# Performance work log

Hardware: AMD Instinct MI355X
Metric: run time of the kernel (lower is better)

Reference implementation:

```python
import jax, jax.numpy as jnp
import numpy as np

INV_SQRT2 = 0.7071067811865476  # db1 (Haar) filter coefficient
KEYS = ("aad", "ada", "add", "daa", "dad", "dda", "ddd")  # ptwt wavedec3 detail keys, dims (D,H,W)


def dwt1(x, axis):
    """Single-level 1D Haar DWT along `axis` (zero mode, even length -> no padding).
    lo[k] = (x[2k] + x[2k+1]) / sqrt(2), hi[k] = (x[2k] - x[2k+1]) / sqrt(2),
    matching pywt/ptwt db1 with mode='zero'."""
    ev = jax.lax.slice_in_dim(x, 0, None, stride=2, axis=axis)
    od = jax.lax.slice_in_dim(x, 1, None, stride=2, axis=axis)
    return (ev + od) * INV_SQRT2, (ev - od) * INV_SQRT2


def haar3(x):
    """One level of separable 3D Haar DWT on [B, C, D, H, W] -> dict of 8 subbands,
    each [B, C, D/2, H/2, W/2]. Key letters correspond to (D, H, W)."""
    out = {}
    aD, dD = dwt1(x, 2)
    for k0, t0 in (("a", aD), ("d", dD)):
        aH, dH = dwt1(t0, 3)
        for k1, t1 in (("a", aH), ("d", dH)):
            aW, dW = dwt1(t1, 4)
            out[k0 + k1 + "a"] = aW
            out[k0 + k1 + "d"] = dW
    return out


def wavedec3(x, level):
    """Multi-level 3D Haar wavedec (ptwt.wavedec3, wavelet='db1', mode='zero').
    Returns (Yl, [details_coarsest, ..., details_finest])."""
    details = []
    cur = x
    for _ in range(level):
        sb = haar3(cur)
        cur = sb.pop("aaa")
        details.append(sb)
    return cur, details[::-1]  # ptwt orders coarsest level first


def setup_inputs() -> dict:
    key = jax.random.key(0)
    x = jax.random.normal(key, (4, 8, 128, 128, 128), dtype=jnp.float32)
    return {"x": x, "level": 5}


def reference(x, level):
    Yl, Yh = wavedec3(x, level)
    outs = [Yl]
    for d in Yh:
        outs.extend(d[k] for k in KEYS)
    return tuple(outs)
```

## Files before the change

### kernel.cpp

```cpp
#include <hip/hip_runtime.h>


#define C3 0.3535533905932738f

typedef float f4 __attribute__((ext_vector_type(4)));

__device__ __forceinline__ f4 ntload(const float* p) {
    return __builtin_nontemporal_load((const f4*)p);
}
__device__ __forceinline__ void ntstore(float* p, f4 v) {
    __builtin_nontemporal_store(v, (f4*)p);
}

__device__ __forceinline__ void haar_quad(const float r[4][8], float o[8][4]) {
#pragma unroll
    for (int j = 0; j < 4; ++j) {
        const float aw0 = r[0][2*j] + r[0][2*j+1], dw0 = r[0][2*j] - r[0][2*j+1];
        const float aw1 = r[1][2*j] + r[1][2*j+1], dw1 = r[1][2*j] - r[1][2*j+1];
        const float aw2 = r[2][2*j] + r[2][2*j+1], dw2 = r[2][2*j] - r[2][2*j+1];
        const float aw3 = r[3][2*j] + r[3][2*j+1], dw3 = r[3][2*j] - r[3][2*j+1];
        const float aa0 = aw0 + aw1, da0 = aw0 - aw1, ad0 = dw0 + dw1, dd0 = dw0 - dw1;
        const float aa1 = aw2 + aw3, da1 = aw2 - aw3, ad1 = dw2 + dw3, dd1 = dw2 - dw3;
        o[0][j] = (aa0 + aa1) * C3;
        o[1][j] = (ad0 + ad1) * C3;
        o[2][j] = (da0 + da1) * C3;
        o[3][j] = (dd0 + dd1) * C3;
        o[4][j] = (aa0 - aa1) * C3;
        o[5][j] = (ad0 - ad1) * C3;
        o[6][j] = (da0 - da1) * C3;
        o[7][j] = (dd0 - dd1) * C3;
    }
}

__device__ __forceinline__ void lds_quad(const float* p, int dh, int dd, float r[4][8]) {
    *(f4*)&r[0][0] = *(const f4*)(p);
    *(f4*)&r[0][4] = *(const f4*)(p + 4);
    *(f4*)&r[1][0] = *(const f4*)(p + dh);
    *(f4*)&r[1][4] = *(const f4*)(p + dh + 4);
    *(f4*)&r[2][0] = *(const f4*)(p + dd);
    *(f4*)&r[2][4] = *(const f4*)(p + dd + 4);
    *(f4*)&r[3][0] = *(const f4*)(p + dd + dh);
    *(f4*)&r[3][4] = *(const f4*)(p + dd + dh + 4);
}

__global__ __launch_bounds__(512, 4) void haar3_fused(
    const float* __restrict__ in, float* __restrict__ out)
{
    __shared__ float A1[16 * 16 * 68];
    __shared__ float A2[8 * 8 * 36];
    __shared__ float A3[4 * 4 * 16];
    __shared__ float A4[2 * 2 * 8];

    const int tid = threadIdx.x;
    const int bc = blockIdx.x >> 4;
    const int db = (blockIdx.x >> 2) & 3;
    const int hb = blockIdx.x & 3;

    const float* xin = in + (((long)bc * 128 + db * 32) * 128 + hb * 32) * 128;
    float* const d1 = out + 8388608;
    float* const d2 = out + 1048576;
    float* const d3 = out + 131072;
    float* const d4 = out + 16384;
    float* const d5 = out + 2048;

    for (int it = 0; it < 8; ++it) {
        const int u = it * 512 + tid;
        const int wg = u & 15, hy = (u >> 4) & 15, dz = u >> 8;
        const float* p = xin + ((long)(2 * dz) * 128 + 2 * hy) * 128 + 8 * wg;
        float r[4][8];
        *(f4*)&r[0][0] = ntload(p);
        *(f4*)&r[0][4] = ntload(p + 4);
        *(f4*)&r[1][0] = ntload(p + 128);
        *(f4*)&r[1][4] = ntload(p + 132);
        *(f4*)&r[2][0] = ntload(p + 16384);
        *(f4*)&r[2][4] = ntload(p + 16388);
        *(f4*)&r[3][0] = ntload(p + 16512);
        *(f4*)&r[3][4] = ntload(p + 16516);
        float o[8][4];
        haar_quad(r, o);
        *(f4*)&A1[(dz * 16 + hy) * 68 + 4 * wg] = *(const f4*)&o[0][0];
        const long di = (((long)bc * 64 + db * 16 + dz) * 64 + hb * 16 + hy) * 64 + 4 * wg;
#pragma unroll
        for (int s = 0; s < 7; ++s)
            ntstore(d1 + (long)s * 8388608 + di, *(const f4*)&o[s + 1][0]);
    }
    __syncthreads();

    {
        const int wg = tid & 7, hy = (tid >> 3) & 7, dz = tid >> 6;
        float r[4][8];
        lds_quad(&A1[((2 * dz) * 16 + 2 * hy) * 68 + 8 * wg], 68, 16 * 68, r);
        float o[8][4];
        haar_quad(r, o);
        *(f4*)&A2[(dz * 8 + hy) * 36 + 4 * wg] = *(const f4*)&o[0][0];
        const long di = (((long)bc * 32 + db * 8 + dz) * 32 + hb * 8 + hy) * 32 + 4 * wg;
#pragma unroll
        for (int s = 0; s < 7; ++s)
            ntstore(d2 + (long)s * 1048576 + di, *(const f4*)&o[s + 1][0]);
    }
    __syncthreads();

    if (tid < 64) {
        const int wg = tid & 3, hy = (tid >> 2) & 3, dz = tid >> 4;
        float r[4][8];
        lds_quad(&A2[((2 * dz) * 8 + 2 * hy) * 36 + 8 * wg], 36, 8 * 36, r);
        float o[8][4];
        haar_quad(r, o);
        *(f4*)&A3[(dz * 4 + hy) * 16 + 4 * wg] = *(const f4*)&o[0][0];
        const long di = (((long)bc * 16 + db * 4 + dz) * 16 + hb * 4 + hy) * 16 + 4 * wg;
#pragma unroll
        for (int s = 0; s < 7; ++s)
            ntstore(d3 + (long)s * 131072 + di, *(const f4*)&o[s + 1][0]);
    }
    __syncthreads();

    if (tid < 8) {
        const int wg = tid & 1, hy = (tid >> 1) & 1, dz = tid >> 2;
        float r[4][8];
        lds_quad(&A3[((2 * dz) * 4 + 2 * hy) * 16 + 8 * wg], 16, 64, r);
        float o[8][4];
        haar_quad(r, o);
        *(f4*)&A4[(dz * 2 + hy) * 8 + 4 * wg] = *(const f4*)&o[0][0];
        const long di = (((long)bc * 8 + db * 2 + dz) * 8 + hb * 2 + hy) * 8 + 4 * wg;
#pragma unroll
        for (int s = 0; s < 7; ++s)
            ntstore(d4 + (long)s * 16384 + di, *(const f4*)&o[s + 1][0]);
    }
    __syncthreads();

    if (tid == 0) {
        float r[4][8];
        lds_quad(&A4[0], 8, 16, r);
        float o[8][4];
        haar_quad(r, o);
        const long di = (((long)bc * 4 + db) * 4 + hb) * 4;
        *(f4*)(out + di) = *(const f4*)&o[0][0];
#pragma unroll
        for (int s = 0; s < 7; ++s)
            *(f4*)(d5 + (long)s * 2048 + di) = *(const f4*)&o[s + 1][0];
    }
}

extern "C" void kernel_launch(void* const* d_in, const int* in_sizes, int n_in,
                              void* d_out, int out_size, void* d_ws, size_t ws_size,
                              hipStream_t stream) {
    const float* x = (const float*)d_in[0];
    float* out = (float*)d_out;
    (void)d_ws; (void)ws_size;

    haar3_fused<<<512, 512, 0, stream>>>(x, out);
}
```

Baseline: 456.6 us.

## Split blocks along W, swizzle level-1 LDS layout, and alias LDS buffers

```diff
diff --git a/kernel.cpp b/kernel.cpp
--- a/kernel.cpp
+++ b/kernel.cpp
@@ -4,6 +4,7 @@
 #define C3 0.3535533905932738f
 
 typedef float f4 __attribute__((ext_vector_type(4)));
+typedef float f2 __attribute__((ext_vector_type(2)));
 
 __device__ __forceinline__ f4 ntload(const float* p) {
     return __builtin_nontemporal_load((const f4*)p);
@@ -32,96 +33,108 @@
     }
 }
 
-__device__ __forceinline__ void lds_quad(const float* p, int dh, int dd, float r[4][8]) {
-    *(f4*)&r[0][0] = *(const f4*)(p);
-    *(f4*)&r[0][4] = *(const f4*)(p + 4);
-    *(f4*)&r[1][0] = *(const f4*)(p + dh);
-    *(f4*)&r[1][4] = *(const f4*)(p + dh + 4);
-    *(f4*)&r[2][0] = *(const f4*)(p + dd);
-    *(f4*)&r[2][4] = *(const f4*)(p + dd + 4);
-    *(f4*)&r[3][0] = *(const f4*)(p + dd + dh);
-    *(f4*)&r[3][4] = *(const f4*)(p + dd + dh + 4);
+__device__ __forceinline__ int sw1(int dz, int hy, int c4) {
+    return (dz * 16 + hy) * 32 + (c4 ^ ((((dz >> 1) ^ (hy >> 1)) & 7) << 2));
 }
 
 __global__ __launch_bounds__(512, 4) void haar3_fused(
     const float* __restrict__ in, float* __restrict__ out)
 {
-    __shared__ float A1[16 * 16 * 68];
-    __shared__ float A2[8 * 8 * 36];
-    __shared__ float A3[4 * 4 * 16];
-    __shared__ float A4[2 * 2 * 8];
+    __shared__ float A1[16 * 16 * 32];
+    __shared__ float A2[8 * 8 * 16];
+    float* const A3 = A1;
+    float* const A4 = A2;
 
     const int tid = threadIdx.x;
-    const int bc = blockIdx.x >> 4;
-    const int db = (blockIdx.x >> 2) & 3;
-    const int hb = blockIdx.x & 3;
+    const int bid = blockIdx.x;
+    const int wb = bid & 1, hb = (bid >> 1) & 3, db = (bid >> 3) & 3, bc = bid >> 5;
 
-    const float* xin = in + (((long)bc * 128 + db * 32) * 128 + hb * 32) * 128;
+    const float* xin = in + (((long)bc * 128 + db * 32) * 128 + hb * 32) * 128 + wb * 64;
     float* const d1 = out + 8388608;
     float* const d2 = out + 1048576;
     float* const d3 = out + 131072;
     float* const d4 = out + 16384;
     float* const d5 = out + 2048;
 
-    for (int it = 0; it < 8; ++it) {
+#pragma unroll 2
+    for (int it = 0; it < 4; ++it) {
         const int u = it * 512 + tid;
-        const int wg = u & 15, hy = (u >> 4) & 15, dz = u >> 8;
+        const int wg = u & 7, hy = (u >> 3) & 15, dz = u >> 7;
         const float* p = xin + ((long)(2 * dz) * 128 + 2 * hy) * 128 + 8 * wg;
         float r[4][8];
-        *(f4*)&r[0][0] = ntload(p);
-        *(f4*)&r[0][4] = ntload(p + 4);
-        *(f4*)&r[1][0] = ntload(p + 128);
-        *(f4*)&r[1][4] = ntload(p + 132);
-        *(f4*)&r[2][0] = ntload(p + 16384);
-        *(f4*)&r[2][4] = ntload(p + 16388);
-        *(f4*)&r[3][0] = ntload(p + 16512);
-        *(f4*)&r[3][4] = ntload(p + 16516);
+        *(f4*)&r[0][0] = ntload(p);         *(f4*)&r[0][4] = ntload(p + 4);
+        *(f4*)&r[1][0] = ntload(p + 128);   *(f4*)&r[1][4] = ntload(p + 132);
+        *(f4*)&r[2][0] = ntload(p + 16384); *(f4*)&r[2][4] = ntload(p + 16388);
+        *(f4*)&r[3][0] = ntload(p + 16512); *(f4*)&r[3][4] = ntload(p + 16516);
         float o[8][4];
         haar_quad(r, o);
-        *(f4*)&A1[(dz * 16 + hy) * 68 + 4 * wg] = *(const f4*)&o[0][0];
-        const long di = (((long)bc * 64 + db * 16 + dz) * 64 + hb * 16 + hy) * 64 + 4 * wg;
+        *(f4*)&A1[sw1(dz, hy, 4 * wg)] = *(const f4*)&o[0][0];
+        const long di = (((long)bc * 64 + db * 16 + dz) * 64 + hb * 16 + hy) * 64
+                        + 32 * wb + 4 * wg;
 #pragma unroll
         for (int s = 0; s < 7; ++s)
             ntstore(d1 + (long)s * 8388608 + di, *(const f4*)&o[s + 1][0]);
     }
     __syncthreads();
 
-    {
-        const int wg = tid & 7, hy = (tid >> 3) & 7, dz = tid >> 6;
+    if (tid < 256) {
+        const int wg = tid & 3, hy = (tid >> 2) & 7, dz = tid >> 5;
         float r[4][8];
-        lds_quad(&A1[((2 * dz) * 16 + 2 * hy) * 68 + 8 * wg], 68, 16 * 68, r);
+#pragma unroll
+        for (int a = 0; a < 2; ++a)
+#pragma unroll
+            for (int b = 0; b < 2; ++b) {
+                *(f4*)&r[a * 2 + b][0] = *(const f4*)&A1[sw1(2*dz + a, 2*hy + b, 8*wg)];
+                *(f4*)&r[a * 2 + b][4] = *(const f4*)&A1[sw1(2*dz + a, 2*hy + b, 8*wg + 4)];
+            }
         float o[8][4];
         haar_quad(r, o);
-        *(f4*)&A2[(dz * 8 + hy) * 36 + 4 * wg] = *(const f4*)&o[0][0];
-        const long di = (((long)bc * 32 + db * 8 + dz) * 32 + hb * 8 + hy) * 32 + 4 * wg;
+        *(f4*)&A2[(dz * 8 + hy) * 16 + 4 * wg] = *(const f4*)&o[0][0];
+        const long di = (((long)bc * 32 + db * 8 + dz) * 32 + hb * 8 + hy) * 32
+                        + 16 * wb + 4 * wg;
 #pragma unroll
         for (int s = 0; s < 7; ++s)
             ntstore(d2 + (long)s * 1048576 + di, *(const f4*)&o[s + 1][0]);
     }
     __syncthreads();
 
-    if (tid < 64) {
-        const int wg = tid & 3, hy = (tid >> 2) & 3, dz = tid >> 4;
+    if (tid < 32) {
+        const int wg = tid & 1, hy = (tid >> 1) & 3, dz = tid >> 3;
         float r[4][8];
-        lds_quad(&A2[((2 * dz) * 8 + 2 * hy) * 36 + 8 * wg], 36, 8 * 36, r);
+#pragma unroll
+        for (int a = 0; a < 2; ++a)
+#pragma unroll
+            for (int b = 0; b < 2; ++b) {
+                const int row = (2 * dz + a) * 8 + 2 * hy + b;
+                *(f4*)&r[a * 2 + b][0] = *(const f4*)&A2[row * 16 + 8 * wg];
+                *(f4*)&r[a * 2 + b][4] = *(const f4*)&A2[row * 16 + 8 * wg + 4];
+            }
         float o[8][4];
         haar_quad(r, o);
-        *(f4*)&A3[(dz * 4 + hy) * 16 + 4 * wg] = *(const f4*)&o[0][0];
-        const long di = (((long)bc * 16 + db * 4 + dz) * 16 + hb * 4 + hy) * 16 + 4 * wg;
+        *(f4*)&A3[(dz * 4 + hy) * 8 + 4 * wg] = *(const f4*)&o[0][0];
+        const long di = (((long)bc * 16 + db * 4 + dz) * 16 + hb * 4 + hy) * 16
+                        + 8 * wb + 4 * wg;
 #pragma unroll
         for (int s = 0; s < 7; ++s)
             ntstore(d3 + (long)s * 131072 + di, *(const f4*)&o[s + 1][0]);
     }
     __syncthreads();
 
-    if (tid < 8) {
-        const int wg = tid & 1, hy = (tid >> 1) & 1, dz = tid >> 2;
+    if (tid < 4) {
+        const int hy = tid & 1, dz = tid >> 1;
         float r[4][8];
-        lds_quad(&A3[((2 * dz) * 4 + 2 * hy) * 16 + 8 * wg], 16, 64, r);
+#pragma unroll
+        for (int a = 0; a < 2; ++a)
+#pragma unroll
+            for (int b = 0; b < 2; ++b) {
+                const int row = (2 * dz + a) * 4 + 2 * hy + b;
+                *(f4*)&r[a * 2 + b][0] = *(const f4*)&A3[row * 8];
+                *(f4*)&r[a * 2 + b][4] = *(const f4*)&A3[row * 8 + 4];
+            }
         float o[8][4];
         haar_quad(r, o);
-        *(f4*)&A4[(dz * 2 + hy) * 8 + 4 * wg] = *(const f4*)&o[0][0];
-        const long di = (((long)bc * 8 + db * 2 + dz) * 8 + hb * 2 + hy) * 8 + 4 * wg;
+        *(f4*)&A4[(dz * 2 + hy) * 4] = *(const f4*)&o[0][0];
+        const long di = (((long)bc * 8 + db * 2 + dz) * 8 + hb * 2 + hy) * 8 + 4 * wb;
 #pragma unroll
         for (int s = 0; s < 7; ++s)
             ntstore(d4 + (long)s * 16384 + di, *(const f4*)&o[s + 1][0]);
@@ -129,15 +142,33 @@
     __syncthreads();
 
     if (tid == 0) {
-        float r[4][8];
-        lds_quad(&A4[0], 8, 16, r);
-        float o[8][4];
-        haar_quad(r, o);
-        const long di = (((long)bc * 4 + db) * 4 + hb) * 4;
-        *(f4*)(out + di) = *(const f4*)&o[0][0];
+        float r[4][4];
+#pragma unroll
+        for (int k = 0; k < 4; ++k)
+            *(f4*)&r[k][0] = *(const f4*)&A4[k * 4];
+        float o[8][2];
+#pragma unroll
+        for (int j = 0; j < 2; ++j) {
+            const float aw0 = r[0][2*j] + r[0][2*j+1], dw0 = r[0][2*j] - r[0][2*j+1];
+            const float aw1 = r[1][2*j] + r[1][2*j+1], dw1 = r[1][2*j] - r[1][2*j+1];
+            const float aw2 = r[2][2*j] + r[2][2*j+1], dw2 = r[2][2*j] - r[2][2*j+1];
+            const float aw3 = r[3][2*j] + r[3][2*j+1], dw3 = r[3][2*j] - r[3][2*j+1];
+            const float aa0 = aw0 + aw1, da0 = aw0 - aw1, ad0 = dw0 + dw1, dd0 = dw0 - dw1;
+            const float aa1 = aw2 + aw3, da1 = aw2 - aw3, ad1 = dw2 + dw3, dd1 = dw2 - dw3;
+            o[0][j] = (aa0 + aa1) * C3;
+            o[1][j] = (ad0 + ad1) * C3;
+            o[2][j] = (da0 + da1) * C3;
+            o[3][j] = (dd0 + dd1) * C3;
+            o[4][j] = (aa0 - aa1) * C3;
+            o[5][j] = (ad0 - ad1) * C3;
+            o[6][j] = (da0 - da1) * C3;
+            o[7][j] = (dd0 - dd1) * C3;
+        }
+        const long di = (((long)bc * 4 + db) * 4 + hb) * 4 + 2 * wb;
+        *(f2*)(out + di) = *(const f2*)&o[0][0];
 #pragma unroll
         for (int s = 0; s < 7; ++s)
-            *(f4*)(d5 + (long)s * 2048 + di) = *(const f4*)&o[s + 1][0];
+            *(f2*)(d5 + (long)s * 2048 + di) = *(const f2*)&o[s + 1][0];
     }
 }
 
@@ -148,5 +179,5 @@
     float* out = (float*)d_out;
     (void)d_ws; (void)ws_size;
 
-    haar3_fused<<<512, 512, 0, stream>>>(x, out);
+    haar3_fused<<<1024, 512, 0, stream>>>(x, out);
 }
```

New measurement: 452.3 us. Within noise of the previous version (-0.9%).
